# Kernel tuning notes

Measured on AMD Instinct MI355X. Metric: run time of the kernel, lower is better.

Reference implementation:

```python
import jax, jax.numpy as jnp
import numpy as np

B, S, HID = 1, 2048, 2048
NH, NKV, HD = 32, 8, 64
INTER = 8192
EPS = 1e-6


def rmsnorm(x, w, eps=EPS):
    xf = x.astype(jnp.float32)
    inv = jax.lax.rsqrt(jnp.mean(xf * xf, axis=-1, keepdims=True) + eps)
    return (xf * inv * w).astype(x.dtype)


def rope(x, sin_t, cos_t):
    # x: [B, S, H, D]; sin/cos: [S, D//2]
    sin = sin_t[None, :, None, :]
    cos = cos_t[None, :, None, :]
    d2 = x.shape[-1] // 2
    x0, x1 = x[..., :d2], x[..., d2:]
    return jnp.concatenate((x0 * cos - x1 * sin, x0 * sin + x1 * cos), axis=-1)


def setup_inputs() -> dict:
    key = jax.random.key(0)
    ks = jax.random.split(key, 12)
    hidden_states = jax.random.normal(ks[0], (B, S, HID), dtype=jnp.float32)
    # realistic RoPE tables
    inv_freq = 1.0 / (10000.0 ** (np.arange(0, HD // 2, dtype=np.float32) * 2.0 / HD))
    ang = np.arange(S, dtype=np.float32)[:, None] * inv_freq[None, :]
    sin_table = jnp.asarray(np.sin(ang))
    cos_table = jnp.asarray(np.cos(ang))
    s = 0.02
    return {
        "hidden_states": hidden_states,
        "sin_table": sin_table,
        "cos_table": cos_table,
        "ln1_w": jnp.ones((HID,), jnp.float32),
        "ln2_w": jnp.ones((HID,), jnp.float32),
        "wq": jax.random.normal(ks[1], (HID, NH * HD), jnp.float32) * s,
        "wk": jax.random.normal(ks[2], (HID, NKV * HD), jnp.float32) * s,
        "wv": jax.random.normal(ks[3], (HID, NKV * HD), jnp.float32) * s,
        "wo": jax.random.normal(ks[4], (NH * HD, HID), jnp.float32) * s,
        "w_gate": jax.random.normal(ks[5], (HID, INTER), jnp.float32) * s,
        "w_up": jax.random.normal(ks[6], (HID, INTER), jnp.float32) * s,
        "w_down": jax.random.normal(ks[7], (INTER, HID), jnp.float32) * s,
    }


def attention(x, sin_t, cos_t, wq, wk, wv, wo):
    b, s, _ = x.shape
    q = (x @ wq).reshape(b, s, NH, HD)
    k = (x @ wk).reshape(b, s, NKV, HD)
    v = (x @ wv).reshape(b, s, NKV, HD).transpose(0, 2, 1, 3)  # [B,Hk,S,D]
    q = rope(q, sin_t, cos_t).transpose(0, 2, 1, 3)  # [B,Hq,S,D]
    k = rope(k, sin_t, cos_t).transpose(0, 2, 1, 3)  # [B,Hk,S,D]
    g = NH // NKV
    k = jnp.repeat(k, g, axis=1)
    v = jnp.repeat(v, g, axis=1)
    scale = 1.0 / np.sqrt(HD)
    scores = jnp.einsum("bhqd,bhkd->bhqk", q, k) * scale
    mask = jnp.tril(jnp.ones((s, s), dtype=bool))
    scores = jnp.where(mask, scores, -jnp.inf)
    probs = jax.nn.softmax(scores, axis=-1)
    out = jnp.einsum("bhqk,bhkd->bhqd", probs, v)
    out = out.transpose(0, 2, 1, 3).reshape(b, s, NH * HD)
    return out @ wo


def reference(hidden_states, sin_table, cos_table, ln1_w, ln2_w, wq, wk, wv, wo, w_gate, w_up, w_down):
    x = hidden_states
    x = x + attention(rmsnorm(x, ln1_w), sin_table, cos_table, wq, wk, wv, wo)
    h = rmsnorm(x, ln2_w)
    x = x + (jax.nn.silu(h @ w_gate) * (h @ w_up)) @ w_down
    return x
```

## Files before the change

### kernel.cpp

```cpp
#include <hip/hip_runtime.h>
#include <hip/hip_bf16.h>

typedef float f32x4 __attribute__((ext_vector_type(4)));
typedef unsigned int u32x4 __attribute__((ext_vector_type(4)));
typedef unsigned int u32x2 __attribute__((ext_vector_type(2)));
typedef _Float16 f16x4 __attribute__((ext_vector_type(4)));
typedef unsigned short u16;

#define S_LEN 2048
#define HID 2048
#define NHEAD 32
#define NKVH 8
#define HDIM 64

__device__ __forceinline__ unsigned short f2bf_bits(float f) {
    unsigned int u = __builtin_bit_cast(unsigned int, f);
    unsigned int r = u + 0x7fffu + ((u >> 16) & 1u);
    return (unsigned short)(r >> 16);
}
__device__ __forceinline__ float bf2f(unsigned short b) {
    unsigned int u = ((unsigned int)b) << 16;
    return __builtin_bit_cast(float, u);
}
__device__ __forceinline__ unsigned cvt_pk_bf16(float lo, float hi) {
    unsigned d;
    asm("v_cvt_pk_bf16_f32 %0, %1, %2" : "=v"(d) : "v"(lo), "v"(hi));
    return d;
}

__device__ __forceinline__ f32x4 mfma_bf16(u32x4 a, u32x4 b, f32x4 c) {
    asm("v_mfma_f32_16x16x32_bf16 %0, %1, %2, %0" : "+v"(c) : "v"(a), "v"(b));
    return c;
}

__device__ __forceinline__ void gload_lds16(const void* g, void* l) {
    __builtin_amdgcn_global_load_lds(
        (const __attribute__((address_space(1))) void*)g,
        (__attribute__((address_space(3))) void*)l, 16, 0, 0);
}

__global__ __launch_bounds__(256)
void rmsnorm_k(const float* __restrict__ x, const float* __restrict__ wgt,
               unsigned short* __restrict__ out)
{
    int row = blockIdx.x;
    int t = threadIdx.x;
    const float* xr = x + (size_t)row * HID;
    f32x4 a = *(const f32x4*)(xr + t * 8);
    f32x4 b = *(const f32x4*)(xr + t * 8 + 4);
    float s = 0.f;
#pragma unroll
    for (int i = 0; i < 4; ++i) s += a[i] * a[i] + b[i] * b[i];
#pragma unroll
    for (int off = 32; off > 0; off >>= 1) s += __shfl_down(s, off);
    __shared__ float red[4];
    if ((t & 63) == 0) red[t >> 6] = s;
    __syncthreads();
    float tot = red[0] + red[1] + red[2] + red[3];
    float inv = rsqrtf(tot * (1.0f / (float)HID) + 1e-6f);
    f32x4 wa = *(const f32x4*)(wgt + t * 8);
    f32x4 wb = *(const f32x4*)(wgt + t * 8 + 4);
    unsigned int pk[4];
#pragma unroll
    for (int i = 0; i < 2; ++i) {
        pk[i]     = (unsigned)f2bf_bits(a[2*i] * inv * wa[2*i]) |
                    ((unsigned)f2bf_bits(a[2*i+1] * inv * wa[2*i+1]) << 16);
        pk[i + 2] = (unsigned)f2bf_bits(b[2*i] * inv * wb[2*i]) |
                    ((unsigned)f2bf_bits(b[2*i+1] * inv * wb[2*i+1]) << 16);
    }
    u32x4 ov; ov[0] = pk[0]; ov[1] = pk[1]; ov[2] = pk[2]; ov[3] = pk[3];
    *(u32x4*)(out + (size_t)row * HID + t * 8) = ov;
}

__global__ __launch_bounds__(256)
void transpose_cvt(const float* __restrict__ in, unsigned short* __restrict__ out,
                   int K, int N)
{
    __shared__ unsigned short tile[64 * 65];
    int kb = blockIdx.y * 64, nb = blockIdx.x * 64;
    int t = threadIdx.x;
    int r = t >> 2, c0 = (t & 3) * 16;
    const float* src = in + (size_t)(kb + r) * N + nb + c0;
#pragma unroll
    for (int j = 0; j < 4; ++j) {
        f32x4 v = *(const f32x4*)(src + j * 4);
#pragma unroll
        for (int i = 0; i < 4; ++i)
            tile[r * 65 + c0 + j * 4 + i] = f2bf_bits(v[i]);
    }
    __syncthreads();
    unsigned short e[16];
#pragma unroll
    for (int j = 0; j < 16; ++j) e[j] = tile[(c0 + j) * 65 + r];
    u32x4 o0, o1;
#pragma unroll
    for (int j = 0; j < 4; ++j) {
        o0[j] = (unsigned)e[2*j] | ((unsigned)e[2*j+1] << 16);
        o1[j] = (unsigned)e[8 + 2*j] | ((unsigned)e[8 + 2*j+1] << 16);
    }
    unsigned short* dst = out + (size_t)(nb + r) * K + kb + c0;
    *(u32x4*)(dst) = o0;
    *(u32x4*)(dst + 8) = o1;
}

__global__ __launch_bounds__(256)
void rope_k(unsigned short* __restrict__ qkv, const float* __restrict__ sin_t,
            const float* __restrict__ cos_t)
{
    int s = blockIdx.x;
    for (int it = threadIdx.x; it < (NHEAD + NKVH) * 32; it += 256) {
        int slot = it >> 5;
        int d = it & 31;
        int col = (slot < NHEAD) ? slot * 64 + d : HID + (slot - NHEAD) * 64 + d;
        unsigned short* p = qkv + (size_t)s * 3072 + col;
        float x0 = bf2f(p[0]);
        float x1 = bf2f(p[32]);
        float c = cos_t[s * 32 + d];
        float sn = sin_t[s * 32 + d];
        p[0]  = f2bf_bits(x0 * c - x1 * sn);
        p[32] = f2bf_bits(x0 * sn + x1 * c);
    }
}

__global__ __launch_bounds__(256)
void transpose_v(const unsigned short* __restrict__ qkv, unsigned short* __restrict__ vT)
{
    __shared__ unsigned short tile[64][80];
    int kb = blockIdx.x * 64, kvh = blockIdx.y;
    int t = threadIdx.x;
    int r = t >> 2, c0 = (t & 3) * 16;
    const unsigned short* src = qkv + (size_t)(kb + r) * 3072 + 2560 + kvh * 64 + c0;
    u32x4 v0 = *(const u32x4*)(src);
    u32x4 v1 = *(const u32x4*)(src + 8);
    *(u32x4*)&tile[r][c0] = v0;
    *(u32x4*)&tile[r][c0 + 8] = v1;
    __syncthreads();
    int d = t >> 2, k0 = (t & 3) * 16;
    unsigned short e[16];
#pragma unroll
    for (int j = 0; j < 16; ++j) e[j] = tile[k0 + j][d];
    u32x4 o0, o1;
#pragma unroll
    for (int j = 0; j < 4; ++j) {
        o0[j] = (unsigned)e[2*j] | ((unsigned)e[2*j+1] << 16);
        o1[j] = (unsigned)e[8 + 2*j] | ((unsigned)e[8 + 2*j+1] << 16);
    }
    int s0 = ((k0 >> 3) ^ (d & 7)) & 7;
    int s1 = (((k0 >> 3) + 1) ^ (d & 7)) & 7;
    unsigned short* dst = vT + ((size_t)kvh * 64 + d) * 2048 + kb;
    *(u32x4*)(dst + s0 * 8) = o0;
    *(u32x4*)(dst + s1 * 8) = o1;
}

template <int EPI>
__global__ __launch_bounds__(256)
void gemm_bt(const unsigned short* __restrict__ A,
             const unsigned short* __restrict__ Bt,
             void* __restrict__ outp, const void* __restrict__ auxp,
             int M, int N, int Kc, int lda)
{
    __shared__ unsigned short As[2][128 * 32];
    __shared__ unsigned short Bs[2][128 * 32];
    int t = threadIdx.x, w = t >> 6, l = t & 63;
    int rb = blockIdx.y, cb = blockIdx.x, zb = blockIdx.z;
    int wr = w >> 1, wc = w & 1;
    int l4 = l >> 4, l15 = l & 15;
    int arow = l >> 2, acol = (l & 3) * 8;
    f32x4 acc[4][4] = {};
    const unsigned short* Ag = A + (size_t)rb * 128 * lda + (size_t)zb * Kc
                                 + (size_t)(w * 16 + arow) * lda + acol;
    const unsigned short* Bg = Bt + (size_t)cb * 128 * lda + (size_t)zb * Kc
                                 + (size_t)(w * 16 + arow) * lda + acol;
    int nk = Kc >> 5;

#define STAGE(buf, kt)                                                          \
    {                                                                           \
        const unsigned short* Agk = Ag + (size_t)(kt) * 32;                     \
        const unsigned short* Bgk = Bg + (size_t)(kt) * 32;                     \
        gload_lds16(Agk, &As[buf][w * 512]);                                    \
        gload_lds16(Agk + (size_t)64 * lda, &As[buf][(4 + w) * 512]);           \
        gload_lds16(Bgk, &Bs[buf][w * 512]);                                    \
        gload_lds16(Bgk + (size_t)64 * lda, &Bs[buf][(4 + w) * 512]);           \
    }

    STAGE(0, 0);
    __syncthreads();
    int cur = 0;
    for (int kt = 0; kt < nk; ++kt) {
        if (kt + 1 < nk) STAGE(cur ^ 1, kt + 1);
        u32x4 af[4], bfr[4];
#pragma unroll
        for (int i = 0; i < 4; ++i)
            af[i] = *(const u32x4*)(&As[cur][(wr * 64 + i * 16 + l15) * 32 + l4 * 8]);
#pragma unroll
        for (int n = 0; n < 4; ++n)
            bfr[n] = *(const u32x4*)(&Bs[cur][(wc * 64 + n * 16 + l15) * 32 + l4 * 8]);
#pragma unroll
        for (int i = 0; i < 4; ++i)
#pragma unroll
            for (int n = 0; n < 4; ++n)
                acc[i][n] = mfma_bf16(af[i], bfr[n], acc[i][n]);
        __syncthreads();
        cur ^= 1;
    }
#undef STAGE

    int row0 = rb * 128 + wr * 64 + l4 * 4;
    int col0 = cb * 128 + wc * 64 + l15;
#pragma unroll
    for (int i = 0; i < 4; ++i) {
#pragma unroll
        for (int n = 0; n < 4; ++n) {
#pragma unroll
            for (int r = 0; r < 4; ++r) {
                int row = row0 + i * 16 + r;
                int col = col0 + n * 16;
                size_t idx = (size_t)row * N + col;
                float v = acc[i][n][r];
                if (EPI == 0) {
                    ((unsigned short*)outp)[idx] = f2bf_bits(v);
                } else if (EPI == 3) {
                    ((float*)outp)[idx] = v + ((const float*)auxp)[idx];
                } else {
                    ((_Float16*)outp)[(size_t)zb * M * N + idx] = (_Float16)v;
                }
            }
        }
    }
}

template <int KK>
__device__ __forceinline__ void phaseP(u16* lds, int cur, f32x4 (&acc)[8][4],
                                       u32x4 (&rcur)[12], u32x4 (&rnext)[12],
                                       int aoff, int boff,
                                       const u16* Asrc, const u16* Bsrc,
                                       int lda, int kt_stage,
                                       int dst0, int dst1)
{
    asm volatile("s_waitcnt vmcnt(4)" ::: "memory");
    {
        int nbuf = (KK == 0) ? cur : (cur ^ 1);
        int nslot = (KK == 0) ? 2 : 0;
        const u16* ah = lds + (nbuf * 4 + nslot) * 8192 + aoff;
        const u16* bh = lds + (nbuf * 4 + nslot + 1) * 8192 + boff;
#pragma unroll
        for (int m = 0; m < 8; ++m)
            rnext[m] = *(const u32x4*)(ah + (m >> 2) * 2048 + (m & 3) * 512);
#pragma unroll
        for (int ni = 0; ni < 4; ++ni)
            rnext[8 + ni] = *(const u32x4*)(bh + ni * 512);
    }
    {
        const u16* sa = Asrc + (size_t)kt_stage * 64 + (KK == 0 ? 32 : 0);
        const u16* sb = Bsrc + (size_t)kt_stage * 64 + (KK == 0 ? 32 : 0);
        int dbuf = (KK == 0) ? (cur ^ 1) : cur;
        u16* dA = lds + (dbuf * 4 + (KK == 0 ? 2 : 0)) * 8192;
        u16* dB = lds + (dbuf * 4 + (KK == 0 ? 3 : 1)) * 8192;
        gload_lds16(sa, dA + dst0);
        gload_lds16(sa + (size_t)128 * lda, dA + dst1);
        gload_lds16(sb, dB + dst0);
        gload_lds16(sb + (size_t)128 * lda, dB + dst1);
    }
    __builtin_amdgcn_sched_barrier(0);
    __builtin_amdgcn_s_setprio(1);
#pragma unroll
    for (int m = 0; m < 8; ++m)
#pragma unroll
        for (int ni = 0; ni < 4; ++ni)
            acc[m][ni] = mfma_bf16(rcur[m], rcur[8 + ni], acc[m][ni]);
    __builtin_amdgcn_s_setprio(0);
    __builtin_amdgcn_s_barrier();
}

template <int EPI>
__global__ __launch_bounds__(512, 2)
void gemm8p(const u16* __restrict__ A, const u16* __restrict__ Bt,
            void* __restrict__ outp, const void* __restrict__ auxp,
            int M, int N, int Kc, int lda)
{
    extern __shared__ u16 lds[];
    const int tid = threadIdx.x;
    const int w = tid >> 6, l = tid & 63;
    const int wm = w >> 2, wn = w & 3;
    const int l4 = l >> 4, l15 = l & 15;
    const int zb = blockIdx.y;

    int wg = blockIdx.x, nwg = gridDim.x;
    int swzb = ((nwg & 7) == 0) ? ((wg & 7) * (nwg >> 3) + (wg >> 3)) : wg;
    int rbs = M >> 8;
    int rb = swzb % rbs, cb = swzb / rbs;

    const int sw = ((tid & 3) ^ ((tid >> 3) & 3)) * 8;
    const int srow = tid >> 2;
    const u16* Asrc = A + (size_t)(rb * 256 + srow) * lda + (size_t)zb * Kc + sw;
    const u16* Bsrc = Bt + (size_t)(cb * 256 + srow) * lda + (size_t)zb * Kc + sw;
    const int dst0 = tid * 8, dst1 = (512 + tid) * 8;

    const int rswz = (l15 >> 1) & 3;
    const int aoff = (wm * 128 + l15) * 32 + (l4 ^ rswz) * 8;
    const int boff = (wn * 64 + l15) * 32 + (l4 ^ rswz) * 8;

    f32x4 acc[8][4] = {};
    u32x4 rA[12], rB[12];
    const int NT = Kc >> 6;

    {
#pragma unroll
        for (int h = 0; h < 2; ++h) {
            const u16* sA = Asrc + h * 32;
            const u16* sB = Bsrc + h * 32;
            gload_lds16(sA, lds + (h * 2) * 8192 + dst0);
            gload_lds16(sA + (size_t)128 * lda, lds + (h * 2) * 8192 + dst1);
            gload_lds16(sB, lds + (h * 2 + 1) * 8192 + dst0);
            gload_lds16(sB + (size_t)128 * lda, lds + (h * 2 + 1) * 8192 + dst1);
        }
        int t1 = (NT > 1) ? 1 : 0;
        const u16* sA = Asrc + (size_t)t1 * 64;
        const u16* sB = Bsrc + (size_t)t1 * 64;
        gload_lds16(sA, lds + (4 + 0) * 8192 + dst0);
        gload_lds16(sA + (size_t)128 * lda, lds + (4 + 0) * 8192 + dst1);
        gload_lds16(sB, lds + (4 + 1) * 8192 + dst0);
        gload_lds16(sB + (size_t)128 * lda, lds + (4 + 1) * 8192 + dst1);
    }
    asm volatile("s_waitcnt vmcnt(8)" ::: "memory");
    __builtin_amdgcn_s_barrier();
    {
        const u16* ah = lds + aoff;
        const u16* bh = lds + 8192 + boff;
#pragma unroll
        for (int m = 0; m < 8; ++m)
            rA[m] = *(const u32x4*)(ah + (m >> 2) * 2048 + (m & 3) * 512);
#pragma unroll
        for (int ni = 0; ni < 4; ++ni)
            rA[8 + ni] = *(const u32x4*)(bh + ni * 512);
    }

    for (int t = 0; t < NT; ++t) {
        int cur = t & 1;
        int k1 = (t + 1 < NT) ? t + 1 : 0;
        int k2 = (t + 2 < NT) ? t + 2 : 0;
        phaseP<0>(lds, cur, acc, rA, rB, aoff, boff, Asrc, Bsrc, lda, k1, dst0, dst1);
        phaseP<1>(lds, cur, acc, rB, rA, aoff, boff, Asrc, Bsrc, lda, k2, dst0, dst1);
    }
    asm volatile("s_waitcnt vmcnt(0)" ::: "memory");

    int row0 = rb * 256 + wm * 128 + l4 * 4;
    int col0 = cb * 256 + wn * 64 + l15;
#pragma unroll
    for (int mi = 0; mi < 8; ++mi) {
#pragma unroll
        for (int ni = 0; ni < 4; ++ni) {
#pragma unroll
            for (int r = 0; r < 4; ++r) {
                int row = row0 + mi * 16 + r;
                int col = col0 + ni * 16;
                size_t idx = (size_t)row * N + col;
                float v = acc[mi][ni][r];
                if (EPI == 1) {
                    float sv = v / (1.0f + __expf(-v));
                    ((unsigned short*)outp)[idx] = f2bf_bits(sv);
                } else if (EPI == 2) {
                    float gv = bf2f(((const unsigned short*)auxp)[idx]);
                    ((unsigned short*)outp)[idx] = f2bf_bits(v * gv);
                } else {
                    ((_Float16*)outp)[(size_t)zb * M * N + idx] = (_Float16)v;
                }
            }
        }
    }
}

template <int KK>
__device__ __forceinline__ void phasePgu(u16* lds, int cur, f32x4 (&acc)[8][4],
                                         u32x4 (&rcur)[12], u32x4 (&rnext)[12],
                                         int aoff, int boffg, int boffu,
                                         const u16* Asrc, const u16* Bg, const u16* Bu,
                                         int lda, int kt_stage,
                                         int dst0, int dst1)
{
    asm volatile("s_waitcnt vmcnt(4)" ::: "memory");
    {
        int nbuf = (KK == 0) ? cur : (cur ^ 1);
        int nslot = (KK == 0) ? 2 : 0;
        const u16* ah = lds + (nbuf * 4 + nslot) * 8192 + aoff;
        const u16* bh = lds + (nbuf * 4 + nslot + 1) * 8192;
#pragma unroll
        for (int m = 0; m < 8; ++m)
            rnext[m] = *(const u32x4*)(ah + (m >> 2) * 2048 + (m & 3) * 512);
#pragma unroll
        for (int ni = 0; ni < 2; ++ni) {
            rnext[8 + ni]  = *(const u32x4*)(bh + boffg + ni * 512);
            rnext[10 + ni] = *(const u32x4*)(bh + boffu + ni * 512);
        }
    }
    {
        int koff = (KK == 0 ? 32 : 0);
        const u16* sa = Asrc + (size_t)kt_stage * 64 + koff;
        int dbuf = (KK == 0) ? (cur ^ 1) : cur;
        u16* dA = lds + (dbuf * 4 + (KK == 0 ? 2 : 0)) * 8192;
        u16* dB = lds + (dbuf * 4 + (KK == 0 ? 3 : 1)) * 8192;
        gload_lds16(sa, dA + dst0);
        gload_lds16(sa + (size_t)128 * lda, dA + dst1);
        gload_lds16(Bg + (size_t)kt_stage * 64 + koff, dB + dst0);
        gload_lds16(Bu + (size_t)kt_stage * 64 + koff, dB + dst1);
    }
    __builtin_amdgcn_sched_barrier(0);
    __builtin_amdgcn_s_setprio(1);
#pragma unroll
    for (int m = 0; m < 8; ++m)
#pragma unroll
        for (int ni = 0; ni < 4; ++ni)
            acc[m][ni] = mfma_bf16(rcur[m], rcur[8 + ni], acc[m][ni]);
    __builtin_amdgcn_s_setprio(0);
    __builtin_amdgcn_s_barrier();
}

__global__ __launch_bounds__(512, 2)
void gemm8p_gu(const u16* __restrict__ A, const u16* __restrict__ WgT,
               const u16* __restrict__ WuT, unsigned short* __restrict__ outp,
               int M, int Nfull, int K)
{
    extern __shared__ u16 lds[];
    const int tid = threadIdx.x;
    const int w = tid >> 6, l = tid & 63;
    const int wm = w >> 2, wn = w & 3;
    const int l4 = l >> 4, l15 = l & 15;

    int wg = blockIdx.x, nwg = gridDim.x;
    int swzb = ((nwg & 7) == 0) ? ((wg & 7) * (nwg >> 3) + (wg >> 3)) : wg;
    int rbs = M >> 8;
    int rb = swzb % rbs, cb = swzb / rbs;

    const int sw = ((tid & 3) ^ ((tid >> 3) & 3)) * 8;
    const int srow = tid >> 2;
    const u16* Asrc = A + (size_t)(rb * 256 + srow) * K + sw;
    const u16* Bg = WgT + (size_t)(cb * 128 + srow) * K + sw;
    const u16* Bu = WuT + (size_t)(cb * 128 + srow) * K + sw;
    const int dst0 = tid * 8, dst1 = (512 + tid) * 8;

    const int rswz = (l15 >> 1) & 3;
    const int aoff  = (wm * 128 + l15) * 32 + (l4 ^ rswz) * 8;
    const int boffg = (wn * 32 + l15) * 32 + (l4 ^ rswz) * 8;
    const int boffu = (128 + wn * 32 + l15) * 32 + (l4 ^ rswz) * 8;

    f32x4 acc[8][4] = {};
    u32x4 rA[12], rB[12];
    const int NT = K >> 6;

    {
#pragma unroll
        for (int h = 0; h < 2; ++h) {
            const u16* sA = Asrc + h * 32;
            gload_lds16(sA, lds + (h * 2) * 8192 + dst0);
            gload_lds16(sA + (size_t)128 * K, lds + (h * 2) * 8192 + dst1);
            gload_lds16(Bg + h * 32, lds + (h * 2 + 1) * 8192 + dst0);
            gload_lds16(Bu + h * 32, lds + (h * 2 + 1) * 8192 + dst1);
        }
        const u16* sA = Asrc + 64;
        gload_lds16(sA, lds + (4 + 0) * 8192 + dst0);
        gload_lds16(sA + (size_t)128 * K, lds + (4 + 0) * 8192 + dst1);
        gload_lds16(Bg + 64, lds + (4 + 1) * 8192 + dst0);
        gload_lds16(Bu + 64, lds + (4 + 1) * 8192 + dst1);
    }
    asm volatile("s_waitcnt vmcnt(8)" ::: "memory");
    __builtin_amdgcn_s_barrier();
    {
        const u16* ah = lds + aoff;
        const u16* bh = lds + 8192;
#pragma unroll
        for (int m = 0; m < 8; ++m)
            rA[m] = *(const u32x4*)(ah + (m >> 2) * 2048 + (m & 3) * 512);
#pragma unroll
        for (int ni = 0; ni < 2; ++ni) {
            rA[8 + ni]  = *(const u32x4*)(bh + boffg + ni * 512);
            rA[10 + ni] = *(const u32x4*)(bh + boffu + ni * 512);
        }
    }

    for (int t = 0; t < NT; ++t) {
        int cur = t & 1;
        int k1 = (t + 1 < NT) ? t + 1 : 0;
        int k2 = (t + 2 < NT) ? t + 2 : 0;
        phasePgu<0>(lds, cur, acc, rA, rB, aoff, boffg, boffu, Asrc, Bg, Bu, K, k1, dst0, dst1);
        phasePgu<1>(lds, cur, acc, rB, rA, aoff, boffg, boffu, Asrc, Bg, Bu, K, k2, dst0, dst1);
    }
    asm volatile("s_waitcnt vmcnt(0)" ::: "memory");

    int row0 = rb * 256 + wm * 128 + l4 * 4;
    int col0 = cb * 128 + wn * 32 + l15;
#pragma unroll
    for (int mi = 0; mi < 8; ++mi) {
#pragma unroll
        for (int ni = 0; ni < 2; ++ni) {
#pragma unroll
            for (int r = 0; r < 4; ++r) {
                int row = row0 + mi * 16 + r;
                int col = col0 + ni * 16;
                float gv = acc[mi][ni][r];
                float uv = acc[mi][ni + 2][r];
                float sv = gv / (1.0f + __expf(-gv)) * uv;
                outp[(size_t)row * Nfull + col] = f2bf_bits(sv);
            }
        }
    }
}

__global__ __launch_bounds__(256)
void reduce_add4(float* __restrict__ out, const _Float16* __restrict__ p, int n)
{
    int i = (blockIdx.x * 256 + threadIdx.x) * 4;
    f32x4 a = *(const f32x4*)(out + i);
#pragma unroll
    for (int z = 0; z < 4; ++z) {
        f16x4 h = *(const f16x4*)(p + (size_t)z * n + i);
#pragma unroll
        for (int j = 0; j < 4; ++j) a[j] += (float)h[j];
    }
    *(f32x4*)(out + i) = a;
}

__global__ __launch_bounds__(256)
void reduce_res4(float* __restrict__ out, const float* __restrict__ x,
                 const _Float16* __restrict__ p, int n)
{
    int i = (blockIdx.x * 256 + threadIdx.x) * 4;
    f32x4 a = *(const f32x4*)(x + i);
#pragma unroll
    for (int z = 0; z < 4; ++z) {
        f16x4 h = *(const f16x4*)(p + (size_t)z * n + i);
#pragma unroll
        for (int j = 0; j < 4; ++j) a[j] += (float)h[j];
    }
    *(f32x4*)(out + i) = a;
}

__global__ __launch_bounds__(256)
void attn_fwd(const unsigned short* __restrict__ qkv,
              const unsigned short* __restrict__ vT,
              unsigned short* __restrict__ out)
{
    int p = blockIdx.x, h = blockIdx.y, kvh = h >> 2;
    int t = threadIdx.x, w = t >> 6, l = t & 63;
    int l4 = l >> 4, l15 = l & 15;
    __shared__ unsigned short Ks[2][64 * 64];
    __shared__ unsigned short Vs[2][64 * 64];

    const unsigned short* Kg = qkv + HID + kvh * 64;
    const unsigned short* Vg = vT + (size_t)kvh * 64 * 2048;

    int ch0 = w * 2, ch1 = w * 2 + 1;
    int rsub = l >> 3;
    int ksw = ((l & 7) ^ (rsub & 7)) * 8;
    int vcol = (l & 7) * 8;
    int sw0 = (l4 ^ (l15 & 7)) * 8;
    int sw1 = ((l4 | 4) ^ (l15 & 7)) * 8;
    int srcA = ((l >> 4) & 1) * 32 + l15;
    int srcB = srcA + 16;
    bool hi32 = (l & 32) != 0;

#define STAGE_KV(buf, kt)                                                         \
    {                                                                             \
        gload_lds16(Kg + (size_t)((kt) * 64 + ch0 * 8 + rsub) * 3072 + ksw,       \
                    &Ks[buf][ch0 * 512]);                                         \
        gload_lds16(Kg + (size_t)((kt) * 64 + ch1 * 8 + rsub) * 3072 + ksw,       \
                    &Ks[buf][ch1 * 512]);                                         \
        gload_lds16(Vg + (size_t)(ch0 * 8 + rsub) * 2048 + (kt) * 64 + vcol,      \
                    &Vs[buf][ch0 * 512]);                                         \
        gload_lds16(Vg + (size_t)(ch1 * 8 + rsub) * 2048 + (kt) * 64 + vcol,      \
                    &Vs[buf][ch1 * 512]);                                         \
    }

    const float SC2 = 0.18033688f;
    const float THR = 44.36f;
    const float BIG = -3.0e38f;

    for (int half = 0; half < 2; ++half) {
        int qb = half ? (31 - p) : p;
        int qrow0 = qb * 64 + w * 16;
        STAGE_KV(0, 0);
        const unsigned short* qg = qkv + (size_t)(qrow0 + l15) * 3072 + h * 64 + l4 * 8;
        u32x4 aq0 = *(const u32x4*)(qg);
        u32x4 aq1 = *(const u32x4*)(qg + 32);
        f32x4 o[4] = {};
        float m = BIG, ls = 0.f;
        __syncthreads();
        int cur = 0;
        for (int kt = 0; kt <= qb; ++kt) {
            if (kt < qb) STAGE_KV(cur ^ 1, kt + 1);
            f32x4 sc[4];
#pragma unroll
            for (int n = 0; n < 4; ++n) {
                const unsigned short* kb_ = &Ks[cur][(n * 16 + l15) * 64];
                u32x4 b0 = *(const u32x4*)(kb_ + sw0);
                u32x4 b1 = *(const u32x4*)(kb_ + sw1);
                f32x4 z = {};
                z = mfma_bf16(b0, aq0, z);
                z = mfma_bf16(b1, aq1, z);
                sc[n] = z;
            }
            if (kt == qb) {
                int qloc = w * 16 + l15;
#pragma unroll
                for (int n = 0; n < 4; ++n)
#pragma unroll
                    for (int r = 0; r < 4; ++r)
                        if (n * 16 + l4 * 4 + r > qloc) sc[n][r] = BIG;
            }
            float rmax = BIG;
#pragma unroll
            for (int n = 0; n < 4; ++n)
#pragma unroll
                for (int r = 0; r < 4; ++r) rmax = fmaxf(rmax, sc[n][r]);
            rmax = fmaxf(rmax, __shfl_xor(rmax, 16));
            rmax = fmaxf(rmax, __shfl_xor(rmax, 32));
            if (__ballot(rmax - m > THR)) {
                float mn = fmaxf(m, rmax);
                float al = __builtin_exp2f((m - mn) * SC2);
                m = mn;
                ls *= al;
#pragma unroll
                for (int nd = 0; nd < 4; ++nd)
#pragma unroll
                    for (int r = 0; r < 4; ++r) o[nd][r] *= al;
            }
            float ms = m * SC2, rs = 0.f;
#pragma unroll
            for (int n = 0; n < 4; ++n)
#pragma unroll
                for (int r = 0; r < 4; ++r) {
                    float pe = __builtin_exp2f(__builtin_fmaf(sc[n][r], SC2, -ms));
                    sc[n][r] = pe;
                    rs += pe;
                }
            rs += __shfl_xor(rs, 16);
            rs += __shfl_xor(rs, 32);
            ls += rs;
            unsigned pk0[2], pk1[2], pk2[2], pk3[2];
#pragma unroll
            for (int rr = 0; rr < 2; ++rr) {
                pk0[rr] = cvt_pk_bf16(sc[0][2*rr], sc[0][2*rr+1]);
                pk1[rr] = cvt_pk_bf16(sc[1][2*rr], sc[1][2*rr+1]);
                pk2[rr] = cvt_pk_bf16(sc[2][2*rr], sc[2][2*rr+1]);
                pk3[rr] = cvt_pk_bf16(sc[3][2*rr], sc[3][2*rr+1]);
            }
            u32x4 W1, W2;
            {
                unsigned a0, a1;
                a0 = __shfl(pk0[0], srcA); a1 = __shfl(pk1[0], srcA); W1[0] = hi32 ? a1 : a0;
                a0 = __shfl(pk0[1], srcA); a1 = __shfl(pk1[1], srcA); W1[1] = hi32 ? a1 : a0;
                a0 = __shfl(pk0[0], srcB); a1 = __shfl(pk1[0], srcB); W1[2] = hi32 ? a1 : a0;
                a0 = __shfl(pk0[1], srcB); a1 = __shfl(pk1[1], srcB); W1[3] = hi32 ? a1 : a0;
                a0 = __shfl(pk2[0], srcA); a1 = __shfl(pk3[0], srcA); W2[0] = hi32 ? a1 : a0;
                a0 = __shfl(pk2[1], srcA); a1 = __shfl(pk3[1], srcA); W2[1] = hi32 ? a1 : a0;
                a0 = __shfl(pk2[0], srcB); a1 = __shfl(pk3[0], srcB); W2[2] = hi32 ? a1 : a0;
                a0 = __shfl(pk2[1], srcB); a1 = __shfl(pk3[1], srcB); W2[3] = hi32 ? a1 : a0;
            }
#pragma unroll
            for (int nd = 0; nd < 4; ++nd) {
                const unsigned short* vb = &Vs[cur][(nd * 16 + l15) * 64];
                u32x4 bv0 = *(const u32x4*)(vb + sw0);
                u32x4 bv1 = *(const u32x4*)(vb + sw1);
                o[nd] = mfma_bf16(bv0, W1, o[nd]);
                o[nd] = mfma_bf16(bv1, W2, o[nd]);
            }
            __syncthreads();
            cur ^= 1;
        }
#undef STAGE_KV
        float linv = 1.0f / ls;
        unsigned short* orow = out + (size_t)(qrow0 + l15) * HID + h * 64 + l4 * 4;
#pragma unroll
        for (int nd = 0; nd < 4; ++nd) {
            u32x2 wv;
            wv[0] = cvt_pk_bf16(o[nd][0] * linv, o[nd][1] * linv);
            wv[1] = cvt_pk_bf16(o[nd][2] * linv, o[nd][3] * linv);
            *(u32x2*)(orow + nd * 16) = wv;
        }
    }
}

extern "C" void kernel_launch(void* const* d_in, const int* in_sizes, int n_in,
                              void* d_out, int out_size, void* d_ws, size_t ws_size,
                              hipStream_t stream)
{
    const float* x     = (const float*)d_in[0];
    const float* sin_t = (const float*)d_in[1];
    const float* cos_t = (const float*)d_in[2];
    const float* ln1w  = (const float*)d_in[3];
    const float* ln2w  = (const float*)d_in[4];
    const float* wq    = (const float*)d_in[5];
    const float* wk    = (const float*)d_in[6];
    const float* wv    = (const float*)d_in[7];
    const float* wo    = (const float*)d_in[8];
    const float* wg    = (const float*)d_in[9];
    const float* wu    = (const float*)d_in[10];
    const float* wd    = (const float*)d_in[11];
    float* out = (float*)d_out;

    char* ws = (char*)d_ws;
    if (ws_size < 113246208u) return;
    unsigned short* wT    = (unsigned short*)(ws);
    unsigned short* xn    = (unsigned short*)(ws + 33554432u);
    unsigned short* qkv   = (unsigned short*)(ws + 41943040u);
    unsigned short* attn  = (unsigned short*)(ws + 54525952u);
    unsigned short* vT    = (unsigned short*)(ws + 62914560u);
    unsigned short* wuT   = (unsigned short*)(ws + 41943040u);
    _Float16*       part  = (_Float16*)(ws + 41943040u);
    unsigned short* g     = (unsigned short*)(ws + 79691776u);
    _Float16*       opart = (_Float16*)(ws + 79691776u);

    hipFuncSetAttribute(reinterpret_cast<const void*>(&gemm8p<5>),
                        hipFuncAttributeMaxDynamicSharedMemorySize, 131072);
    hipFuncSetAttribute(reinterpret_cast<const void*>(&gemm8p_gu),
                        hipFuncAttributeMaxDynamicSharedMemorySize, 131072);

    rmsnorm_k<<<S_LEN, 256, 0, stream>>>(x, ln1w, xn);

    transpose_cvt<<<dim3(32, 32), 256, 0, stream>>>(wq, wT, 2048, 2048);
    transpose_cvt<<<dim3(8, 32), 256, 0, stream>>>(wk, wT + (size_t)2048 * 2048, 2048, 512);
    transpose_cvt<<<dim3(8, 32), 256, 0, stream>>>(wv, wT + (size_t)2560 * 2048, 2048, 512);

    gemm_bt<0><<<dim3(24, 16, 1), 256, 0, stream>>>(xn, wT, qkv, nullptr, 2048, 3072, 2048, 2048);

    rope_k<<<S_LEN, 256, 0, stream>>>(qkv, sin_t, cos_t);
    transpose_v<<<dim3(32, 8), 256, 0, stream>>>(qkv, vT);

    attn_fwd<<<dim3(16, 32), 256, 0, stream>>>(qkv, vT, attn);

    transpose_cvt<<<dim3(32, 32), 256, 0, stream>>>(wo, wT, 2048, 2048);
    gemm8p<5><<<dim3(64, 4), 512, 131072, stream>>>(attn, wT, opart, nullptr, 2048, 2048, 512, 2048);
    reduce_res4<<<4096, 256, 0, stream>>>(out, x, opart, 4194304);

    rmsnorm_k<<<S_LEN, 256, 0, stream>>>(out, ln2w, xn);

    transpose_cvt<<<dim3(128, 32), 256, 0, stream>>>(wg, wT, 2048, 8192);
    transpose_cvt<<<dim3(128, 32), 256, 0, stream>>>(wu, wuT, 2048, 8192);
    gemm8p_gu<<<dim3(512), 512, 131072, stream>>>(xn, wT, wuT, g, 2048, 8192, 2048);

    transpose_cvt<<<dim3(32, 128), 256, 0, stream>>>(wd, wT, 8192, 2048);
    gemm8p<5><<<dim3(64, 4), 512, 131072, stream>>>(g, wT, part, nullptr, 2048, 2048, 2048, 8192);

    reduce_add4<<<4096, 256, 0, stream>>>(out, part, 4194304);
}
```

Measured before the change: 431.5 us.

## Replace LDS-staged split-K GEMM with direct global-to-register MFMA loads

The split-K GEMM used for the o-projection and down-projection no longer stages A/B tiles through LDS with async global-to-LDS copies and barriers. Each wave now loads its MFMA operand fragments straight from global memory into registers, double-buffered across 32-wide K phases. This removes LDS traffic and barrier synchronisation and frees the 128 KB of dynamic LDS. In exchange, operands that neighbouring waves share are re-read from global/L2 instead of being reused from LDS, and the per-lane 16-byte row-strided loads are less coalesced.

```diff
diff --git a/kernel.cpp b/kernel.cpp
--- a/kernel.cpp
+++ b/kernel.cpp
@@ -229,56 +229,12 @@
     }
 }
 
-template <int KK>
-__device__ __forceinline__ void phaseP(u16* lds, int cur, f32x4 (&acc)[8][4],
-                                       u32x4 (&rcur)[12], u32x4 (&rnext)[12],
-                                       int aoff, int boff,
-                                       const u16* Asrc, const u16* Bsrc,
-                                       int lda, int kt_stage,
-                                       int dst0, int dst1)
-{
-    asm volatile("s_waitcnt vmcnt(4)" ::: "memory");
-    {
-        int nbuf = (KK == 0) ? cur : (cur ^ 1);
-        int nslot = (KK == 0) ? 2 : 0;
-        const u16* ah = lds + (nbuf * 4 + nslot) * 8192 + aoff;
-        const u16* bh = lds + (nbuf * 4 + nslot + 1) * 8192 + boff;
-#pragma unroll
-        for (int m = 0; m < 8; ++m)
-            rnext[m] = *(const u32x4*)(ah + (m >> 2) * 2048 + (m & 3) * 512);
-#pragma unroll
-        for (int ni = 0; ni < 4; ++ni)
-            rnext[8 + ni] = *(const u32x4*)(bh + ni * 512);
-    }
-    {
-        const u16* sa = Asrc + (size_t)kt_stage * 64 + (KK == 0 ? 32 : 0);
-        const u16* sb = Bsrc + (size_t)kt_stage * 64 + (KK == 0 ? 32 : 0);
-        int dbuf = (KK == 0) ? (cur ^ 1) : cur;
-        u16* dA = lds + (dbuf * 4 + (KK == 0 ? 2 : 0)) * 8192;
-        u16* dB = lds + (dbuf * 4 + (KK == 0 ? 3 : 1)) * 8192;
-        gload_lds16(sa, dA + dst0);
-        gload_lds16(sa + (size_t)128 * lda, dA + dst1);
-        gload_lds16(sb, dB + dst0);
-        gload_lds16(sb + (size_t)128 * lda, dB + dst1);
-    }
-    __builtin_amdgcn_sched_barrier(0);
-    __builtin_amdgcn_s_setprio(1);
-#pragma unroll
-    for (int m = 0; m < 8; ++m)
-#pragma unroll
-        for (int ni = 0; ni < 4; ++ni)
-            acc[m][ni] = mfma_bf16(rcur[m], rcur[8 + ni], acc[m][ni]);
-    __builtin_amdgcn_s_setprio(0);
-    __builtin_amdgcn_s_barrier();
-}
-
 template <int EPI>
 __global__ __launch_bounds__(512, 2)
-void gemm8p(const u16* __restrict__ A, const u16* __restrict__ Bt,
-            void* __restrict__ outp, const void* __restrict__ auxp,
-            int M, int N, int Kc, int lda)
-{
-    extern __shared__ u16 lds[];
+void gemm_dr(const u16* __restrict__ A, const u16* __restrict__ Bt,
+             void* __restrict__ outp, const void* __restrict__ auxp,
+             int M, int N, int Kc, int lda)
+{
     const int tid = threadIdx.x;
     const int w = tid >> 6, l = tid & 63;
     const int wm = w >> 2, wn = w & 3;
@@ -290,59 +246,45 @@
     int rbs = M >> 8;
     int rb = swzb % rbs, cb = swzb / rbs;
 
-    const int sw = ((tid & 3) ^ ((tid >> 3) & 3)) * 8;
-    const int srow = tid >> 2;
-    const u16* Asrc = A + (size_t)(rb * 256 + srow) * lda + (size_t)zb * Kc + sw;
-    const u16* Bsrc = Bt + (size_t)(cb * 256 + srow) * lda + (size_t)zb * Kc + sw;
-    const int dst0 = tid * 8, dst1 = (512 + tid) * 8;
-
-    const int rswz = (l15 >> 1) & 3;
-    const int aoff = (wm * 128 + l15) * 32 + (l4 ^ rswz) * 8;
-    const int boff = (wn * 64 + l15) * 32 + (l4 ^ rswz) * 8;
+    const u16* Abase = A + (size_t)(rb * 256 + wm * 128 + l15) * lda
+                         + (size_t)zb * Kc + l4 * 8;
+    const u16* Bbase = Bt + (size_t)(cb * 256 + wn * 64 + l15) * lda
+                         + (size_t)zb * Kc + l4 * 8;
 
     f32x4 acc[8][4] = {};
     u32x4 rA[12], rB[12];
-    const int NT = Kc >> 6;
-
-    {
-#pragma unroll
-        for (int h = 0; h < 2; ++h) {
-            const u16* sA = Asrc + h * 32;
-            const u16* sB = Bsrc + h * 32;
-            gload_lds16(sA, lds + (h * 2) * 8192 + dst0);
-            gload_lds16(sA + (size_t)128 * lda, lds + (h * 2) * 8192 + dst1);
-            gload_lds16(sB, lds + (h * 2 + 1) * 8192 + dst0);
-            gload_lds16(sB + (size_t)128 * lda, lds + (h * 2 + 1) * 8192 + dst1);
-        }
-        int t1 = (NT > 1) ? 1 : 0;
-        const u16* sA = Asrc + (size_t)t1 * 64;
-        const u16* sB = Bsrc + (size_t)t1 * 64;
-        gload_lds16(sA, lds + (4 + 0) * 8192 + dst0);
-        gload_lds16(sA + (size_t)128 * lda, lds + (4 + 0) * 8192 + dst1);
-        gload_lds16(sB, lds + (4 + 1) * 8192 + dst0);
-        gload_lds16(sB + (size_t)128 * lda, lds + (4 + 1) * 8192 + dst1);
-    }
-    asm volatile("s_waitcnt vmcnt(8)" ::: "memory");
-    __builtin_amdgcn_s_barrier();
-    {
-        const u16* ah = lds + aoff;
-        const u16* bh = lds + 8192 + boff;
-#pragma unroll
-        for (int m = 0; m < 8; ++m)
-            rA[m] = *(const u32x4*)(ah + (m >> 2) * 2048 + (m & 3) * 512);
-#pragma unroll
-        for (int ni = 0; ni < 4; ++ni)
-            rA[8 + ni] = *(const u32x4*)(bh + ni * 512);
-    }
-
-    for (int t = 0; t < NT; ++t) {
-        int cur = t & 1;
-        int k1 = (t + 1 < NT) ? t + 1 : 0;
-        int k2 = (t + 2 < NT) ? t + 2 : 0;
-        phaseP<0>(lds, cur, acc, rA, rB, aoff, boff, Asrc, Bsrc, lda, k1, dst0, dst1);
-        phaseP<1>(lds, cur, acc, rB, rA, aoff, boff, Asrc, Bsrc, lda, k2, dst0, dst1);
-    }
-    asm volatile("s_waitcnt vmcnt(0)" ::: "memory");
+    const int NP = Kc >> 5;
+
+#define LOADPH(dst, ph)                                                         \
+    {                                                                           \
+        int ko = (ph) * 32;                                                     \
+        _Pragma("unroll")                                                       \
+        for (int mi = 0; mi < 8; ++mi)                                          \
+            dst[mi] = *(const u32x4*)(Abase + (size_t)mi * 16 * lda + ko);      \
+        _Pragma("unroll")                                                       \
+        for (int ni = 0; ni < 4; ++ni)                                          \
+            dst[8 + ni] = *(const u32x4*)(Bbase + (size_t)ni * 16 * lda + ko);  \
+    }
+#define MFMABLK(src)                                                            \
+    {                                                                           \
+        __builtin_amdgcn_s_setprio(1);                                          \
+        _Pragma("unroll")                                                       \
+        for (int mi = 0; mi < 8; ++mi)                                          \
+            _Pragma("unroll")                                                   \
+            for (int ni = 0; ni < 4; ++ni)                                      \
+                acc[mi][ni] = mfma_bf16(src[mi], src[8 + ni], acc[mi][ni]);     \
+        __builtin_amdgcn_s_setprio(0);                                          \
+    }
+
+    LOADPH(rA, 0);
+    for (int p = 0; p < NP; p += 2) {
+        LOADPH(rB, (p + 1 < NP) ? p + 1 : 0);
+        MFMABLK(rA);
+        LOADPH(rA, (p + 2 < NP) ? p + 2 : 0);
+        MFMABLK(rB);
+    }
+#undef LOADPH
+#undef MFMABLK
 
     int row0 = rb * 256 + wm * 128 + l4 * 4;
     int col0 = cb * 256 + wn * 64 + l15;
@@ -355,16 +297,7 @@
                 int row = row0 + mi * 16 + r;
                 int col = col0 + ni * 16;
                 size_t idx = (size_t)row * N + col;
-                float v = acc[mi][ni][r];
-                if (EPI == 1) {
-                    float sv = v / (1.0f + __expf(-v));
-                    ((unsigned short*)outp)[idx] = f2bf_bits(sv);
-                } else if (EPI == 2) {
-                    float gv = bf2f(((const unsigned short*)auxp)[idx]);
-                    ((unsigned short*)outp)[idx] = f2bf_bits(v * gv);
-                } else {
-                    ((_Float16*)outp)[(size_t)zb * M * N + idx] = (_Float16)v;
-                }
+                ((_Float16*)outp)[(size_t)zb * M * N + idx] = (_Float16)acc[mi][ni][r];
             }
         }
     }
@@ -709,8 +642,6 @@
     unsigned short* g     = (unsigned short*)(ws + 79691776u);
     _Float16*       opart = (_Float16*)(ws + 79691776u);
 
-    hipFuncSetAttribute(reinterpret_cast<const void*>(&gemm8p<5>),
-                        hipFuncAttributeMaxDynamicSharedMemorySize, 131072);
     hipFuncSetAttribute(reinterpret_cast<const void*>(&gemm8p_gu),
                         hipFuncAttributeMaxDynamicSharedMemorySize, 131072);
 
@@ -728,7 +659,7 @@
     attn_fwd<<<dim3(16, 32), 256, 0, stream>>>(qkv, vT, attn);
 
     transpose_cvt<<<dim3(32, 32), 256, 0, stream>>>(wo, wT, 2048, 2048);
-    gemm8p<5><<<dim3(64, 4), 512, 131072, stream>>>(attn, wT, opart, nullptr, 2048, 2048, 512, 2048);
+    gemm_dr<5><<<dim3(64, 4), 512, 0, stream>>>(attn, wT, opart, nullptr, 2048, 2048, 512, 2048);
     reduce_res4<<<4096, 256, 0, stream>>>(out, x, opart, 4194304);
 
     rmsnorm_k<<<S_LEN, 256, 0, stream>>>(out, ln2w, xn);
@@ -738,7 +669,7 @@
     gemm8p_gu<<<dim3(512), 512, 131072, stream>>>(xn, wT, wuT, g, 2048, 8192, 2048);
 
     transpose_cvt<<<dim3(32, 128), 256, 0, stream>>>(wd, wT, 8192, 2048);
-    gemm8p<5><<<dim3(64, 4), 512, 131072, stream>>>(g, wT, part, nullptr, 2048, 2048, 2048, 8192);
+    gemm_dr<5><<<dim3(64, 4), 512, 0, stream>>>(g, wT, part, nullptr, 2048, 2048, 2048, 8192);
 
     reduce_add4<<<4096, 256, 0, stream>>>(out, part, 4194304);
 }
```

Result: slower. 568.2 us (+31.7%).
